# Kernel tuning notes

Measured on AMD Instinct MI355X. Metric: run time of the kernel, lower is better.

Reference implementation:

```python
import jax, jax.numpy as jnp
import numpy as np

B, S, D = 8, 2048, 768

def setup_inputs() -> dict:
    key = jax.random.key(0)
    kx, kq, kk, kv = jax.random.split(key, 4)
    scale = 1.0 / np.sqrt(D)
    x = jax.random.normal(kx, (B, S, D), dtype=jnp.float32)
    # nn.Linear weights: [out, in], applied as x @ W.T
    Wq = jax.random.normal(kq, (D, D), dtype=jnp.float32) * scale
    Wk = jax.random.normal(kk, (D, D), dtype=jnp.float32) * scale
    Wv = jax.random.normal(kv, (D, D), dtype=jnp.float32) * scale
    return {"x": x, "Wq": Wq, "Wk": Wk, "Wv": Wv}

def reference(x, Wq, Wk, Wv):
    d_k = x.shape[-1]
    Q = jnp.einsum('bsd,ed->bse', x, Wq)
    K = jnp.einsum('bsd,ed->bse', x, Wk)
    V = jnp.einsum('bsd,ed->bse', x, Wv)
    scores = jnp.einsum('bqd,bkd->bqk', Q, K) / jnp.sqrt(jnp.float32(d_k))
    attention_weights = jax.nn.softmax(scores, axis=-1)  # [B,S,S]
    weighted_values = jnp.einsum('bqk,bkd->bqd', attention_weights, V)
    return (weighted_values, attention_weights)
```

## Files before the change

kernel.cpp:

```cpp
#include <hip/hip_runtime.h>
#include <cmath>


typedef __bf16 v8bf __attribute__((ext_vector_type(8)));
typedef float  v4f  __attribute__((ext_vector_type(4)));
typedef unsigned short u16;

__device__ __forceinline__ u16 f2bf(float f) {
  union { float f; unsigned u; } v; v.f = f;
  unsigned r = v.u + 0x7fffu + ((v.u >> 16) & 1u);
  return (u16)(r >> 16);
}

__device__ __forceinline__ uint4 pack8(const float* __restrict__ src) {
  float4 f0 = *(const float4*)src;
  float4 f1 = *(const float4*)(src + 4);
  union { uint4 u; u16 h[8]; } pk;
  pk.h[0] = f2bf(f0.x); pk.h[1] = f2bf(f0.y); pk.h[2] = f2bf(f0.z); pk.h[3] = f2bf(f0.w);
  pk.h[4] = f2bf(f1.x); pk.h[5] = f2bf(f1.y); pk.h[6] = f2bf(f1.z); pk.h[7] = f2bf(f1.w);
  return pk.u;
}

__device__ __forceinline__ void gl_lds16(const void* g, void* l) {
  __builtin_amdgcn_global_load_lds(
      (const __attribute__((address_space(1))) unsigned*)g,
      (__attribute__((address_space(3))) unsigned*)l, 16, 0, 0);
}

enum { OUT_F32 = 0, OUT_QKV = 1 };

constexpr int BM = 128, BN = 128, BK = 64;

template <bool A_F32, int MODE>
__global__ __launch_bounds__(256)
void gemm128(const void* __restrict__ Ag_, const void* __restrict__ Bg_,
             void* __restrict__ C0, void* __restrict__ C1, void* __restrict__ C2,
             int K, int lda, int ldb, int ldc,
             long long sA, long long sB, long long sC, float alpha) {
  __shared__ u16 As[BM * BK];
  __shared__ u16 Bs[BN * BK];

  const int z  = blockIdx.z;
  const int m0 = blockIdx.x * BM;
  const int n0 = blockIdx.y * BN;

  const int t    = threadIdx.x;
  const int lane = t & 63;
  const int w    = t >> 6;
  const int wm   = (w & 1) * 64;
  const int wn   = (w >> 1) * 64;
  const int fr   = lane & 15;
  const int quad = lane >> 4;

  const u16* Bp = (const u16*)Bg_ + (size_t)z * (size_t)sB;

  v4f acc[4][4];
#pragma unroll
  for (int i = 0; i < 4; ++i)
#pragma unroll
    for (int j = 0; j < 4; ++j) acc[i][j] = (v4f){0.f, 0.f, 0.f, 0.f};

  for (int kt = 0; kt < K; kt += BK) {
#pragma unroll
    for (int j = 0; j < 4; ++j) {
      const int s   = (w * 4 + j) * 64 + lane;
      const int row = s >> 3;
      const int gc  = (s & 7) ^ (row & 7);
      gl_lds16(Bp + (size_t)(n0 + row) * ldb + kt + gc * 8, &Bs[s * 8]);
    }
    if constexpr (A_F32) {
      const float* Ap = (const float*)Ag_ + (size_t)z * (size_t)sA;
#pragma unroll
      for (int j = 0; j < 4; ++j) {
        const int g   = j * 256 + t;
        const int row = g >> 3, gc = g & 7;
        const int s   = (g & ~7) | (gc ^ (row & 7));
        uint4 pk = pack8(Ap + (size_t)(m0 + row) * lda + kt + gc * 8);
        *(uint4*)&As[s * 8] = pk;
      }
    } else {
      const u16* Ap = (const u16*)Ag_ + (size_t)z * (size_t)sA;
#pragma unroll
      for (int j = 0; j < 4; ++j) {
        const int s   = (w * 4 + j) * 64 + lane;
        const int row = s >> 3;
        const int gc  = (s & 7) ^ (row & 7);
        gl_lds16(Ap + (size_t)(m0 + row) * lda + kt + gc * 8, &As[s * 8]);
      }
    }
    __syncthreads();

#pragma unroll
    for (int kk = 0; kk < BK; kk += 32) {
      const int kc = (kk >> 3) + quad;
      v8bf af[4], bv[4];
#pragma unroll
      for (int i = 0; i < 4; ++i) {
        const int ra = wm + i * 16 + fr;
        const int rb = wn + i * 16 + fr;
        af[i] = *(const v8bf*)&As[(ra * 8 + (kc ^ (fr & 7))) * 8];
        bv[i] = *(const v8bf*)&Bs[(rb * 8 + (kc ^ (fr & 7))) * 8];
      }
#pragma unroll
      for (int mi = 0; mi < 4; ++mi)
#pragma unroll
        for (int ni = 0; ni < 4; ++ni)
          acc[mi][ni] =
              __builtin_amdgcn_mfma_f32_16x16x32_bf16(af[mi], bv[ni], acc[mi][ni], 0, 0, 0);
    }
    __syncthreads();
  }

  const int r0 = (lane >> 4) * 4;
#pragma unroll
  for (int mi = 0; mi < 4; ++mi) {
#pragma unroll
    for (int ni = 0; ni < 4; ++ni) {
      v4f v = acc[mi][ni];
      const int grow0 = m0 + wm + mi * 16 + r0;
      const int gcol  = n0 + wn + ni * 16 + fr;
      if constexpr (MODE == OUT_F32) {
        float* C = (float*)C0 + (size_t)z * (size_t)sC;
#pragma unroll
        for (int r = 0; r < 4; ++r)
          C[(size_t)(grow0 + r) * ldc + gcol] = v[r] * alpha;
      } else {
        const int grp  = n0 / 768;
        const int lcol = gcol - grp * 768;
        if (grp == 0) {
          u16* C = (u16*)C0;
#pragma unroll
          for (int r = 0; r < 4; ++r)
            C[(size_t)(grow0 + r) * 768 + lcol] = f2bf(v[r]);
        } else if (grp == 1) {
          u16* C = (u16*)C1;
#pragma unroll
          for (int r = 0; r < 4; ++r)
            C[(size_t)(grow0 + r) * 768 + lcol] = f2bf(v[r]);
        } else {
          u16* C = (u16*)C2;
          size_t base = (size_t)(grow0 >> 11) * (768ull * 2048ull) +
                        (size_t)lcol * 2048ull + (size_t)(grow0 & 2047);
          ushort4 st;
          st.x = f2bf(v[0]); st.y = f2bf(v[1]); st.z = f2bf(v[2]); st.w = f2bf(v[3]);
          *(ushort4*)&C[base] = st;
        }
      }
    }
  }
}

__global__ __launch_bounds__(256)
void cvt_bf16(const float* __restrict__ src, u16* __restrict__ dst, int n8) {
  const int i = blockIdx.x * 256 + threadIdx.x;
  if (i < n8) *(uint4*)(dst + (size_t)i * 8) = pack8(src + (size_t)i * 8);
}

__global__ __launch_bounds__(256)
void cvt3_bf16(const float* __restrict__ s0, const float* __restrict__ s1,
               const float* __restrict__ s2, u16* __restrict__ d0,
               u16* __restrict__ d1, u16* __restrict__ d2, int n8) {
  const float* s = blockIdx.y == 0 ? s0 : blockIdx.y == 1 ? s1 : s2;
  u16*         d = blockIdx.y == 0 ? d0 : blockIdx.y == 1 ? d1 : d2;
  const int i = blockIdx.x * 256 + threadIdx.x;
  if (i < n8) *(uint4*)(d + (size_t)i * 8) = pack8(s + (size_t)i * 8);
}

template <bool EMIT>
__global__ __launch_bounds__(256) void softmax_rows(float* __restrict__ w,
                                                    u16* __restrict__ pb) {
  float* p = w + (size_t)blockIdx.x * 2048;
  const int t = threadIdx.x;
  float4 a = *(float4*)(p + t * 4);
  float4 b = *(float4*)(p + 1024 + t * 4);

  float mx = fmaxf(fmaxf(fmaxf(a.x, a.y), fmaxf(a.z, a.w)),
                   fmaxf(fmaxf(b.x, b.y), fmaxf(b.z, b.w)));
#pragma unroll
  for (int off = 32; off; off >>= 1) mx = fmaxf(mx, __shfl_xor(mx, off));
  __shared__ float red[4];
  const int wid = t >> 6, ln = t & 63;
  if (ln == 0) red[wid] = mx;
  __syncthreads();
  mx = fmaxf(fmaxf(red[0], red[1]), fmaxf(red[2], red[3]));

  a.x = __expf(a.x - mx); a.y = __expf(a.y - mx);
  a.z = __expf(a.z - mx); a.w = __expf(a.w - mx);
  b.x = __expf(b.x - mx); b.y = __expf(b.y - mx);
  b.z = __expf(b.z - mx); b.w = __expf(b.w - mx);

  float s = a.x + a.y + a.z + a.w + b.x + b.y + b.z + b.w;
#pragma unroll
  for (int off = 32; off; off >>= 1) s += __shfl_xor(s, off);
  __syncthreads();
  if (ln == 0) red[wid] = s;
  __syncthreads();
  s = red[0] + red[1] + red[2] + red[3];

  const float inv = 1.0f / s;
  a.x *= inv; a.y *= inv; a.z *= inv; a.w *= inv;
  b.x *= inv; b.y *= inv; b.z *= inv; b.w *= inv;
  *(float4*)(p + t * 4) = a;
  *(float4*)(p + 1024 + t * 4) = b;

  if constexpr (EMIT) {
    u16* q = pb + (size_t)blockIdx.x * 2048;
    ushort4 ha, hb;
    ha.x = f2bf(a.x); ha.y = f2bf(a.y); ha.z = f2bf(a.z); ha.w = f2bf(a.w);
    hb.x = f2bf(b.x); hb.y = f2bf(b.y); hb.z = f2bf(b.z); hb.w = f2bf(b.w);
    *(ushort4*)(q + t * 4) = ha;
    *(ushort4*)(q + 1024 + t * 4) = hb;
  }
}

extern "C" void kernel_launch(void* const* d_in, const int* in_sizes, int n_in,
                              void* d_out, int out_size, void* d_ws, size_t ws_size,
                              hipStream_t stream) {
  const float* x  = (const float*)d_in[0];
  const float* Wq = (const float*)d_in[1];
  const float* Wk = (const float*)d_in[2];
  const float* Wv = (const float*)d_in[3];
  float* out = (float*)d_out;
  float* wts = out + 8ull * 2048 * 768;

  u16* Qb  = (u16*)d_out;
  u16* Kb  = Qb + 16384ull * 768;
  u16* xb  = (u16*)wts;
  u16* Wqb = xb + 16384ull * 768;
  u16* Wkb = Wqb + 768ull * 768;
  u16* Wvb = Wkb + 768ull * 768;
  u16* Vt  = (u16*)d_ws;
  u16* Pb  = Vt + 8ull * 768 * 2048;

  const size_t VT_BYTES = 8ull * 768 * 2048 * 2;
  const size_t PB_BYTES = 8ull * 2048 * 2048 * 2;
  const bool   pb_ok    = ws_size >= VT_BYTES + PB_BYTES;

  const dim3 blk(256, 1, 1);
  const float isq = 1.0f / sqrtf(768.0f);

  cvt_bf16<<<dim3(6144, 1, 1), blk, 0, stream>>>(x, xb, 16384 * 768 / 8);
  cvt3_bf16<<<dim3(288, 3, 1), blk, 0, stream>>>(Wq, Wk, Wv, Wqb, Wkb, Wvb,
                                                 768 * 768 / 8);

  gemm128<false, OUT_QKV><<<dim3(128, 18, 1), blk, 0, stream>>>(
      xb, Wqb, (void*)Qb, (void*)Kb, (void*)Vt, 768, 768, 768, 768,
      0, 0, 0, 1.0f);

  gemm128<false, OUT_F32><<<dim3(16, 16, 8), blk, 0, stream>>>(
      Qb, Kb, (void*)wts, nullptr, nullptr, 768, 768, 768, 2048,
      2048ll * 768, 2048ll * 768, 2048ll * 2048, isq);

  if (pb_ok) {
    softmax_rows<true><<<dim3(16384, 1, 1), blk, 0, stream>>>(wts, Pb);
    gemm128<false, OUT_F32><<<dim3(16, 6, 8), blk, 0, stream>>>(
        Pb, Vt, (void*)out, nullptr, nullptr, 2048, 2048, 2048, 768,
        2048ll * 2048, 768ll * 2048, 2048ll * 768, 1.0f);
  } else {
    softmax_rows<false><<<dim3(16384, 1, 1), blk, 0, stream>>>(wts, nullptr);
    gemm128<true, OUT_F32><<<dim3(16, 6, 8), blk, 0, stream>>>(
        wts, Vt, (void*)out, nullptr, nullptr, 2048, 2048, 2048, 768,
        2048ll * 2048, 768ll * 2048, 2048ll * 768, 1.0f);
  }
}
```

Baseline: 448.6 us.

## Store attention scores as bf16 in workspace and merge conversion kernels

The QK^T GEMM now writes its scaled scores as bf16 into a new workspace buffer instead of fp32 into the output weights region. The softmax reads these bf16 scores and writes the fp32 weights plus the bf16 probabilities. This halves the score write and the softmax read traffic, but the softmax input loses precision through bf16 rounding of the logits. The x and weight fp32-to-bf16 conversions are also merged into one launch. The new path runs only if the workspace can hold the extra buffer.

```diff
diff --git a/kernel.cpp b/kernel.cpp
--- a/kernel.cpp
+++ b/kernel.cpp
@@ -10,6 +10,11 @@
   union { float f; unsigned u; } v; v.f = f;
   unsigned r = v.u + 0x7fffu + ((v.u >> 16) & 1u);
   return (u16)(r >> 16);
+}
+
+__device__ __forceinline__ float bf2f(u16 h) {
+  union { unsigned u; float f; } v; v.u = ((unsigned)h) << 16;
+  return v.f;
 }
 
 __device__ __forceinline__ uint4 pack8(const float* __restrict__ src) {
@@ -27,7 +32,7 @@
       (__attribute__((address_space(3))) unsigned*)l, 16, 0, 0);
 }
 
-enum { OUT_F32 = 0, OUT_QKV = 1 };
+enum { OUT_F32 = 0, OUT_QKV = 1, OUT_BF16S = 2 };
 
 constexpr int BM = 128, BN = 128, BK = 64;
 
@@ -124,6 +129,11 @@
 #pragma unroll
         for (int r = 0; r < 4; ++r)
           C[(size_t)(grow0 + r) * ldc + gcol] = v[r] * alpha;
+      } else if constexpr (MODE == OUT_BF16S) {
+        u16* C = (u16*)C0 + (size_t)z * (size_t)sC;
+#pragma unroll
+        for (int r = 0; r < 4; ++r)
+          C[(size_t)(grow0 + r) * ldc + gcol] = f2bf(v[r] * alpha);
       } else {
         const int grp  = n0 / 768;
         const int lcol = gcol - grp * 768;
@@ -151,28 +161,43 @@
 }
 
 __global__ __launch_bounds__(256)
-void cvt_bf16(const float* __restrict__ src, u16* __restrict__ dst, int n8) {
+void cvt_all(const float* __restrict__ x, const float* __restrict__ Wq,
+             const float* __restrict__ Wk, const float* __restrict__ Wv,
+             u16* __restrict__ xb, u16* __restrict__ Wqb,
+             u16* __restrict__ Wkb, u16* __restrict__ Wvb) {
+  constexpr int NX = 16384 * 768 / 8;
+  constexpr int NW = 768 * 768 / 8;
   const int i = blockIdx.x * 256 + threadIdx.x;
-  if (i < n8) *(uint4*)(dst + (size_t)i * 8) = pack8(src + (size_t)i * 8);
-}
-
+  const float* s; u16* d; int idx;
+  if (i < NX) {
+    s = x; d = xb; idx = i;
+  } else {
+    const int j = i - NX;
+    const int g = j / NW;
+    idx = j - g * NW;
+    s = g == 0 ? Wq : g == 1 ? Wk : Wv;
+    d = g == 0 ? Wqb : g == 1 ? Wkb : Wvb;
+  }
+  *(uint4*)(d + (size_t)idx * 8) = pack8(s + (size_t)idx * 8);
+}
+
+template <bool EMIT, bool BF16IN>
 __global__ __launch_bounds__(256)
-void cvt3_bf16(const float* __restrict__ s0, const float* __restrict__ s1,
-               const float* __restrict__ s2, u16* __restrict__ d0,
-               u16* __restrict__ d1, u16* __restrict__ d2, int n8) {
-  const float* s = blockIdx.y == 0 ? s0 : blockIdx.y == 1 ? s1 : s2;
-  u16*         d = blockIdx.y == 0 ? d0 : blockIdx.y == 1 ? d1 : d2;
-  const int i = blockIdx.x * 256 + threadIdx.x;
-  if (i < n8) *(uint4*)(d + (size_t)i * 8) = pack8(s + (size_t)i * 8);
-}
-
-template <bool EMIT>
-__global__ __launch_bounds__(256) void softmax_rows(float* __restrict__ w,
-                                                    u16* __restrict__ pb) {
+void softmax_rows(float* __restrict__ w, u16* __restrict__ pb,
+                  const u16* __restrict__ sb) {
   float* p = w + (size_t)blockIdx.x * 2048;
   const int t = threadIdx.x;
-  float4 a = *(float4*)(p + t * 4);
-  float4 b = *(float4*)(p + 1024 + t * 4);
+  float4 a, b;
+  if constexpr (BF16IN) {
+    const u16* q = sb + (size_t)blockIdx.x * 2048;
+    ushort4 ra = *(const ushort4*)(q + t * 4);
+    ushort4 rb = *(const ushort4*)(q + 1024 + t * 4);
+    a.x = bf2f(ra.x); a.y = bf2f(ra.y); a.z = bf2f(ra.z); a.w = bf2f(ra.w);
+    b.x = bf2f(rb.x); b.y = bf2f(rb.y); b.z = bf2f(rb.z); b.w = bf2f(rb.w);
+  } else {
+    a = *(float4*)(p + t * 4);
+    b = *(float4*)(p + 1024 + t * 4);
+  }
 
   float mx = fmaxf(fmaxf(fmaxf(a.x, a.y), fmaxf(a.z, a.w)),
                    fmaxf(fmaxf(b.x, b.y), fmaxf(b.z, b.w)));
@@ -231,33 +256,47 @@
   u16* Wvb = Wkb + 768ull * 768;
   u16* Vt  = (u16*)d_ws;
   u16* Pb  = Vt + 8ull * 768 * 2048;
+  u16* Sb  = Pb + 8ull * 2048 * 2048;
 
   const size_t VT_BYTES = 8ull * 768 * 2048 * 2;
   const size_t PB_BYTES = 8ull * 2048 * 2048 * 2;
+  const size_t SB_BYTES = PB_BYTES;
   const bool   pb_ok    = ws_size >= VT_BYTES + PB_BYTES;
+  const bool   sb_ok    = ws_size >= VT_BYTES + PB_BYTES + SB_BYTES;
 
   const dim3 blk(256, 1, 1);
   const float isq = 1.0f / sqrtf(768.0f);
 
-  cvt_bf16<<<dim3(6144, 1, 1), blk, 0, stream>>>(x, xb, 16384 * 768 / 8);
-  cvt3_bf16<<<dim3(288, 3, 1), blk, 0, stream>>>(Wq, Wk, Wv, Wqb, Wkb, Wvb,
-                                                 768 * 768 / 8);
+  cvt_all<<<dim3(7008, 1, 1), blk, 0, stream>>>(x, Wq, Wk, Wv,
+                                                xb, Wqb, Wkb, Wvb);
 
   gemm128<false, OUT_QKV><<<dim3(128, 18, 1), blk, 0, stream>>>(
       xb, Wqb, (void*)Qb, (void*)Kb, (void*)Vt, 768, 768, 768, 768,
       0, 0, 0, 1.0f);
 
-  gemm128<false, OUT_F32><<<dim3(16, 16, 8), blk, 0, stream>>>(
-      Qb, Kb, (void*)wts, nullptr, nullptr, 768, 768, 768, 2048,
-      2048ll * 768, 2048ll * 768, 2048ll * 2048, isq);
-
-  if (pb_ok) {
-    softmax_rows<true><<<dim3(16384, 1, 1), blk, 0, stream>>>(wts, Pb);
+  if (sb_ok) {
+    gemm128<false, OUT_BF16S><<<dim3(16, 16, 8), blk, 0, stream>>>(
+        Qb, Kb, (void*)Sb, nullptr, nullptr, 768, 768, 768, 2048,
+        2048ll * 768, 2048ll * 768, 2048ll * 2048, isq);
+    softmax_rows<true, true><<<dim3(16384, 1, 1), blk, 0, stream>>>(wts, Pb, Sb);
+    gemm128<false, OUT_F32><<<dim3(16, 6, 8), blk, 0, stream>>>(
+        Pb, Vt, (void*)out, nullptr, nullptr, 2048, 2048, 2048, 768,
+        2048ll * 2048, 768ll * 2048, 2048ll * 768, 1.0f);
+  } else if (pb_ok) {
+    gemm128<false, OUT_F32><<<dim3(16, 16, 8), blk, 0, stream>>>(
+        Qb, Kb, (void*)wts, nullptr, nullptr, 768, 768, 768, 2048,
+        2048ll * 768, 2048ll * 768, 2048ll * 2048, isq);
+    softmax_rows<true, false><<<dim3(16384, 1, 1), blk, 0, stream>>>(wts, Pb,
+                                                                     nullptr);
     gemm128<false, OUT_F32><<<dim3(16, 6, 8), blk, 0, stream>>>(
         Pb, Vt, (void*)out, nullptr, nullptr, 2048, 2048, 2048, 768,
         2048ll * 2048, 768ll * 2048, 2048ll * 768, 1.0f);
   } else {
-    softmax_rows<false><<<dim3(16384, 1, 1), blk, 0, stream>>>(wts, nullptr);
+    gemm128<false, OUT_F32><<<dim3(16, 16, 8), blk, 0, stream>>>(
+        Qb, Kb, (void*)wts, nullptr, nullptr, 768, 768, 768, 2048,
+        2048ll * 768, 2048ll * 768, 2048ll * 2048, isq);
+    softmax_rows<false, false><<<dim3(16384, 1, 1), blk, 0, stream>>>(
+        wts, nullptr, nullptr);
     gemm128<true, OUT_F32><<<dim3(16, 6, 8), blk, 0, stream>>>(
         wts, Vt, (void*)out, nullptr, nullptr, 2048, 2048, 2048, 768,
         2048ll * 2048, 768ll * 2048, 2048ll * 768, 1.0f);
```

Result: no change. 450.6 us (+0.4%).
